# Performance work log

Hardware: AMD Instinct MI355X
Metric: run time of the kernel (lower is better)

Reference implementation:

```python
import jax, jax.numpy as jnp
import numpy as np

N_NODES = 10000
IN_CH = 128
HID = 256
OUT_CH = 1
N_EDGES_ADJ = 320000  # avg degree 32
N_TARGET = 8192


def setup_inputs() -> dict:
    key = jax.random.key(0)
    ks = jax.random.split(key, 16)
    s = 0.05  # weight scale for numerical stability
    inp = {
        'x': jax.random.normal(ks[0], (N_NODES, IN_CH), jnp.float32),
        'adj_row': jax.random.randint(ks[1], (N_EDGES_ADJ,), 0, N_NODES),
        'adj_col': jax.random.randint(ks[2], (N_EDGES_ADJ,), 0, N_NODES),
        'tar_ei': jax.random.randint(ks[3], (2, N_TARGET), 0, N_NODES),
        'beta': jnp.ones((1,), jnp.float32),
        'W1': s * jax.random.normal(ks[4], (IN_CH, HID), jnp.float32),
        'b1': jnp.zeros((HID,), jnp.float32),
        'W2': s * jax.random.normal(ks[5], (HID, HID), jnp.float32),
        'b2': jnp.zeros((HID,), jnp.float32),
        'W3': s * jax.random.normal(ks[6], (HID, HID), jnp.float32),
        'b3': jnp.zeros((HID,), jnp.float32),
        'Wij1': s * jax.random.normal(ks[7], (IN_CH, HID), jnp.float32),
        'bij1': jnp.zeros((HID,), jnp.float32),
        'Wij2': s * jax.random.normal(ks[8], (HID, HID), jnp.float32),
        'bij2': jnp.zeros((HID,), jnp.float32),
        'Wl1': s * jax.random.normal(ks[9], (HID, HID), jnp.float32),
        'bl1': jnp.zeros((HID,), jnp.float32),
        'Wl2': s * jax.random.normal(ks[10], (HID, OUT_CH), jnp.float32),
        'bl2': jnp.zeros((OUT_CH,), jnp.float32),
    }
    return inp


def reference(x, adj_row, adj_col, tar_ei, beta, W1, b1, W2, b2, W3, b3,
              Wij1, bij1, Wij2, bij2, Wl1, bl1, Wl2, bl2):
    n = x.shape[0]
    # Binary adjacency (duplicates collapse to 1, matching SparseTensor semantics)
    A = jnp.zeros((n, n), x.dtype).at[adj_row, adj_col].set(1.0)
    xi = x[tar_ei[0]]  # [E, F]
    xj = x[tar_ei[1]]  # [E, F]
    # adjoverlap: common-neighbor indicator per target edge, then spmm_add with x
    cn_mask = A[tar_ei[0]] * A[tar_ei[1]]          # [E, N]
    cn_x = cn_mask @ x                              # [E, F] sum of features over common neighbors
    # xcnlin: Linear-ReLU-Linear-ReLU-Linear (eval mode: dropout=identity, ln=identity)
    xcn = jax.nn.relu(cn_x @ W1 + b1)
    xcn = jax.nn.relu(xcn @ W2 + b2)
    xcn = xcn @ W3 + b3
    # xijlin: Linear-ReLU-Linear
    xij = jax.nn.relu((xi * xj) @ Wij1 + bij1) @ Wij2 + bij2
    # lin head: Linear-ReLU-Linear
    h = jax.nn.relu((xcn * beta + xij) @ Wl1 + bl1)
    return h @ Wl2 + bl2  # [E, 1]
```

## Files before the change

kernel.cpp:

```cpp
#include <hip/hip_runtime.h>
#include <hip/hip_bf16.h>

#define N_NODES 10000
#define IN_CH 128
#define HID 256
#define E_TAR 8192
#define N_EDGES 320000
#define WPR 320
#define WUSED 313
#define MAXCN 256
#define MASK_WORDS (N_NODES * WPR)

typedef short bf16x8 __attribute__((ext_vector_type(8)));
typedef float f32x4 __attribute__((ext_vector_type(4)));

__device__ __forceinline__ unsigned short f2bf(float f) {
  union { float f; unsigned u; } v; v.f = f;
  unsigned r = v.u + 0x7fffu + ((v.u >> 16) & 1u);
  return (unsigned short)(r >> 16);
}

__global__ void fill_zero(uint4* __restrict__ p, int n4) {
  int i = blockIdx.x * 256 + threadIdx.x;
  int stride = gridDim.x * 256;
  uint4 z = {0u, 0u, 0u, 0u};
  for (; i < n4; i += stride) p[i] = z;
}

__global__ void scatter_adj(const int* __restrict__ row, const int* __restrict__ col,
                            unsigned* __restrict__ mask) {
  int k = blockIdx.x * 256 + threadIdx.x;
  if (k < N_EDGES) {
    int r = row[k], c = col[k];
    atomicOr(&mask[(size_t)r * WPR + (c >> 5)], 1u << (c & 31));
  }
}

__global__ void cn_gather(const unsigned* __restrict__ mask, const int* __restrict__ tar,
                          const float* __restrict__ x, float* __restrict__ cnx) {
  __shared__ int cnt;
  __shared__ int list[MAXCN];
  int e = blockIdx.x;
  int i = tar[e], j = tar[E_TAR + e];
  if (threadIdx.x == 0) cnt = 0;
  __syncthreads();
  const unsigned* mi = mask + (size_t)i * WPR;
  const unsigned* mj = mask + (size_t)j * WPR;
  for (int w = threadIdx.x; w < WUSED; w += 128) {
    unsigned v = mi[w] & mj[w];
    while (v) {
      int b = __ffs(v) - 1;
      v &= v - 1;
      int pos = atomicAdd(&cnt, 1);
      if (pos < MAXCN) list[pos] = w * 32 + b;
    }
  }
  __syncthreads();
  int n = cnt; if (n > MAXCN) n = MAXCN;
  int c = threadIdx.x;
  float acc = 0.f;
  for (int t = 0; t < n; ++t) acc += x[(size_t)list[t] * IN_CH + c];
  cnx[(size_t)e * IN_CH + c] = acc;
}

__global__ __launch_bounds__(256) void gemm_mfma(
    const float* __restrict__ A, const float* __restrict__ W,
    const float* __restrict__ bias, const float* __restrict__ extra,
    const float* __restrict__ scalePtr, const int* __restrict__ tar,
    const float* __restrict__ x, int relu, int M, int N, int K,
    float* __restrict__ C)
{
  __shared__ unsigned short As[64][56];
  __shared__ unsigned short Bs[64][56];
  int m0 = blockIdx.x * 64;
  int n0 = blockIdx.y * 64;
  int tid = threadIdx.x;
  int lane = tid & 63, wv = tid >> 6;
  int wm0 = (wv >> 1) * 32, wn0 = (wv & 1) * 32;
  f32x4 acc[2][2] = {};

  int arow = tid >> 2, akb = (tid & 3) * 8;
  int bn = tid & 63, bkb = (tid >> 6) * 8;
  int gi = 0, gj = 0;
  if (tar) { gi = tar[m0 + arow]; gj = tar[E_TAR + m0 + arow]; }

  for (int k0 = 0; k0 < K; k0 += 32) {
    float av[8];
    if (tar) {
      const float* xi = x + (size_t)gi * IN_CH + k0 + akb;
      const float* xj = x + (size_t)gj * IN_CH + k0 + akb;
      #pragma unroll
      for (int u = 0; u < 8; ++u) av[u] = xi[u] * xj[u];
    } else {
      const float* ap = A + (size_t)(m0 + arow) * K + k0 + akb;
      #pragma unroll
      for (int u = 0; u < 8; ++u) av[u] = ap[u];
    }
    unsigned short abf[8];
    #pragma unroll
    for (int u = 0; u < 8; ++u) abf[u] = f2bf(av[u]);
    *(bf16x8*)&As[arow][akb] = *(bf16x8*)abf;

    unsigned short bbf[8];
    #pragma unroll
    for (int u = 0; u < 8; ++u) bbf[u] = f2bf(W[(size_t)(k0 + bkb + u) * N + n0 + bn]);
    *(bf16x8*)&Bs[bn][bkb] = *(bf16x8*)bbf;
    __syncthreads();

    int l15 = lane & 15, kq = (lane >> 4) * 8;
    bf16x8 a0 = *(bf16x8*)&As[wm0 + l15][kq];
    bf16x8 a1 = *(bf16x8*)&As[wm0 + 16 + l15][kq];
    bf16x8 b0 = *(bf16x8*)&Bs[wn0 + l15][kq];
    bf16x8 b1 = *(bf16x8*)&Bs[wn0 + 16 + l15][kq];
    acc[0][0] = __builtin_amdgcn_mfma_f32_16x16x32_bf16(a0, b0, acc[0][0], 0, 0, 0);
    acc[0][1] = __builtin_amdgcn_mfma_f32_16x16x32_bf16(a0, b1, acc[0][1], 0, 0, 0);
    acc[1][0] = __builtin_amdgcn_mfma_f32_16x16x32_bf16(a1, b0, acc[1][0], 0, 0, 0);
    acc[1][1] = __builtin_amdgcn_mfma_f32_16x16x32_bf16(a1, b1, acc[1][1], 0, 0, 0);
    __syncthreads();
  }

  float scale = scalePtr ? scalePtr[0] : 0.f;
  int l15 = lane & 15, rq = (lane >> 4) * 4;
  #pragma unroll
  for (int fm = 0; fm < 2; ++fm) {
    #pragma unroll
    for (int fn = 0; fn < 2; ++fn) {
      int cg = n0 + wn0 + fn * 16 + l15;
      float bv = bias[cg];
      #pragma unroll
      for (int i2 = 0; i2 < 4; ++i2) {
        int rg = m0 + wm0 + fm * 16 + rq + i2;
        float v = acc[fm][fn][i2] + bv;
        if (extra) v += scale * extra[(size_t)rg * N + cg];
        if (relu) v = fmaxf(v, 0.f);
        C[(size_t)rg * N + cg] = v;
      }
    }
  }
}

__global__ void final_dot(const float* __restrict__ h, const float* __restrict__ w2,
                          const float* __restrict__ b2, float* __restrict__ out) {
  int wv = threadIdx.x >> 6, lane = threadIdx.x & 63;
  int row = blockIdx.x * 4 + wv;
  const float* hr = h + (size_t)row * HID;
  float s = 0.f;
  #pragma unroll
  for (int t = 0; t < 4; ++t) s += hr[lane + 64 * t] * w2[lane + 64 * t];
  #pragma unroll
  for (int off = 32; off; off >>= 1) s += __shfl_down(s, off);
  if (lane == 0) out[row] = s + b2[0];
}

extern "C" void kernel_launch(void* const* d_in, const int* in_sizes, int n_in,
                              void* d_out, int out_size, void* d_ws, size_t ws_size,
                              hipStream_t stream) {
  const float* x      = (const float*)d_in[0];
  const int*   adj_r  = (const int*)d_in[1];
  const int*   adj_c  = (const int*)d_in[2];
  const int*   tar    = (const int*)d_in[3];
  const float* beta   = (const float*)d_in[4];
  const float* W1     = (const float*)d_in[5];
  const float* b1     = (const float*)d_in[6];
  const float* W2     = (const float*)d_in[7];
  const float* b2     = (const float*)d_in[8];
  const float* W3     = (const float*)d_in[9];
  const float* b3     = (const float*)d_in[10];
  const float* Wij1   = (const float*)d_in[11];
  const float* bij1   = (const float*)d_in[12];
  const float* Wij2   = (const float*)d_in[13];
  const float* bij2   = (const float*)d_in[14];
  const float* Wl1    = (const float*)d_in[15];
  const float* bl1    = (const float*)d_in[16];
  const float* Wl2    = (const float*)d_in[17];
  const float* bl2    = (const float*)d_in[18];

  char* ws = (char*)d_ws;
  unsigned* mask = (unsigned*)ws;
  float* bufA = (float*)(ws + (size_t)16 * 1024 * 1024);
  float* bufB = (float*)(ws + (size_t)24 * 1024 * 1024);
  float* bufC = (float*)(ws + (size_t)32 * 1024 * 1024);

  fill_zero<<<3200, 256, 0, stream>>>((uint4*)mask, MASK_WORDS / 4);
  scatter_adj<<<(N_EDGES + 255) / 256, 256, 0, stream>>>(adj_r, adj_c, mask);
  cn_gather<<<E_TAR, 128, 0, stream>>>(mask, tar, x, bufA);

  dim3 g(E_TAR / 64, HID / 64);
  gemm_mfma<<<g, 256, 0, stream>>>(bufA, W1, b1, nullptr, nullptr, nullptr, nullptr, 1, E_TAR, HID, IN_CH, bufB);
  gemm_mfma<<<g, 256, 0, stream>>>(bufB, W2, b2, nullptr, nullptr, nullptr, nullptr, 1, E_TAR, HID, HID, bufC);
  gemm_mfma<<<g, 256, 0, stream>>>(bufC, W3, b3, nullptr, nullptr, nullptr, nullptr, 0, E_TAR, HID, HID, bufB);
  gemm_mfma<<<g, 256, 0, stream>>>(nullptr, Wij1, bij1, nullptr, nullptr, tar, x, 1, E_TAR, HID, IN_CH, bufC);
  gemm_mfma<<<g, 256, 0, stream>>>(bufC, Wij2, bij2, bufB, beta, nullptr, nullptr, 0, E_TAR, HID, HID, bufA);
  gemm_mfma<<<g, 256, 0, stream>>>(bufA, Wl1, bl1, nullptr, nullptr, nullptr, nullptr, 1, E_TAR, HID, HID, bufC);
  final_dot<<<E_TAR / 4, 256, 0, stream>>>(bufC, Wl2, bl2, (float*)d_out);
}
```

Measured before the change: 88.32 us.

## Fuse MLP chain into one kernel and use CSR-based common-neighbor gathering

Replaces the six separate GEMM launches and the final dot with one fused kernel that keeps 32-row activation tiles in shared memory as bf16 across all layers. Weights are pre-transposed and converted to bf16 once per call. The common-neighbor step now builds a per-row CSR from the bitmask and probes the larger-degree node's bitmask for each neighbor of the smaller one, with one wave per target edge. This removes global round-trips of intermediate activations and the full-row bitmask scans, but adds a CSR build pass and keeps intermediates in bf16.

```diff
diff --git a/kernel.cpp b/kernel.cpp
--- a/kernel.cpp
+++ b/kernel.cpp
@@ -8,16 +8,21 @@
 #define N_EDGES 320000
 #define WPR 320
 #define WUSED 313
-#define MAXCN 256
 #define MASK_WORDS (N_NODES * WPR)
+#define CSR_MAX 128
+#define BM 32
 
 typedef short bf16x8 __attribute__((ext_vector_type(8)));
+typedef short bf16x4 __attribute__((ext_vector_type(4)));
 typedef float f32x4 __attribute__((ext_vector_type(4)));
 
 __device__ __forceinline__ unsigned short f2bf(float f) {
   union { float f; unsigned u; } v; v.f = f;
   unsigned r = v.u + 0x7fffu + ((v.u >> 16) & 1u);
   return (unsigned short)(r >> 16);
+}
+__device__ __forceinline__ float bf2f(unsigned short h) {
+  union { unsigned u; float f; } v; v.u = ((unsigned)h) << 16; return v.f;
 }
 
 __global__ void fill_zero(uint4* __restrict__ p, int n4) {
@@ -36,120 +41,282 @@
   }
 }
 
-__global__ void cn_gather(const unsigned* __restrict__ mask, const int* __restrict__ tar,
-                          const float* __restrict__ x, float* __restrict__ cnx) {
-  __shared__ int cnt;
-  __shared__ int list[MAXCN];
-  int e = blockIdx.x;
-  int i = tar[e], j = tar[E_TAR + e];
-  if (threadIdx.x == 0) cnt = 0;
-  __syncthreads();
-  const unsigned* mi = mask + (size_t)i * WPR;
-  const unsigned* mj = mask + (size_t)j * WPR;
-  for (int w = threadIdx.x; w < WUSED; w += 128) {
-    unsigned v = mi[w] & mj[w];
+__global__ void csr_build(const unsigned* __restrict__ mask, int* __restrict__ deg,
+                          int* __restrict__ csr) {
+  int row = blockIdx.x * 4 + (threadIdx.x >> 6);
+  int lane = threadIdx.x & 63;
+  const unsigned* mr = mask + (size_t)row * WPR;
+  unsigned words[5];
+  int cnt = 0;
+  #pragma unroll
+  for (int t = 0; t < 5; ++t) {
+    int w = lane + 64 * t;
+    unsigned v = (w < WUSED) ? mr[w] : 0u;
+    words[t] = v;
+    cnt += __popc(v);
+  }
+  int pre = cnt;
+  #pragma unroll
+  for (int off = 1; off < 64; off <<= 1) {
+    int n2 = __shfl_up(pre, off);
+    if (lane >= off) pre += n2;
+  }
+  int excl = pre - cnt;
+  int total = __shfl(pre, 63);
+  if (lane == 0) deg[row] = total;
+  int p = excl;
+  int* dst = csr + (size_t)row * CSR_MAX;
+  #pragma unroll
+  for (int t = 0; t < 5; ++t) {
+    unsigned v = words[t];
+    int wbase = (lane + 64 * t) * 32;
     while (v) {
       int b = __ffs(v) - 1;
       v &= v - 1;
-      int pos = atomicAdd(&cnt, 1);
-      if (pos < MAXCN) list[pos] = w * 32 + b;
-    }
-  }
-  __syncthreads();
-  int n = cnt; if (n > MAXCN) n = MAXCN;
-  int c = threadIdx.x;
-  float acc = 0.f;
-  for (int t = 0; t < n; ++t) acc += x[(size_t)list[t] * IN_CH + c];
-  cnx[(size_t)e * IN_CH + c] = acc;
-}
-
-__global__ __launch_bounds__(256) void gemm_mfma(
-    const float* __restrict__ A, const float* __restrict__ W,
-    const float* __restrict__ bias, const float* __restrict__ extra,
-    const float* __restrict__ scalePtr, const int* __restrict__ tar,
-    const float* __restrict__ x, int relu, int M, int N, int K,
-    float* __restrict__ C)
+      if (p < CSR_MAX) dst[p] = wbase + b;
+      ++p;
+    }
+  }
+}
+
+__global__ void cn_gather_csr(const unsigned* __restrict__ mask, const int* __restrict__ deg,
+                              const int* __restrict__ csr, const int* __restrict__ tar,
+                              const float* __restrict__ x, float* __restrict__ cnx) {
+  __shared__ int lists[4][256];
+  __shared__ int cnts[4];
+  int wv = threadIdx.x >> 6, lane = threadIdx.x & 63;
+  int e = blockIdx.x * 4 + wv;
+  int i = tar[e], j = tar[E_TAR + e];
+  int di = deg[i], dj = deg[j];
+  int a = (di <= dj) ? i : j;
+  int b = (di <= dj) ? j : i;
+  int da = min(di, dj);
+  if (lane == 0) cnts[wv] = 0;
+  __syncthreads();
+  const unsigned* mb = mask + (size_t)b * WPR;
+  if (da <= CSR_MAX) {
+    const int* la = csr + (size_t)a * CSR_MAX;
+    for (int t = lane; t < da; t += 64) {
+      int n = la[t];
+      if ((mb[n >> 5] >> (n & 31)) & 1u) {
+        int p = atomicAdd(&cnts[wv], 1);
+        lists[wv][p] = n;
+      }
+    }
+  } else {
+    const unsigned* ma = mask + (size_t)a * WPR;
+    for (int w = lane; w < WUSED; w += 64) {
+      unsigned v = ma[w] & mb[w];
+      while (v) {
+        int bit = __ffs(v) - 1;
+        v &= v - 1;
+        int p = atomicAdd(&cnts[wv], 1);
+        if (p < 256) lists[wv][p] = w * 32 + bit;
+      }
+    }
+  }
+  __syncthreads();
+  int n = cnts[wv]; if (n > 256) n = 256;
+  float a0 = 0.f, a1 = 0.f;
+  for (int t = 0; t < n; ++t) {
+    const float* xr = x + (size_t)lists[wv][t] * IN_CH;
+    a0 += xr[lane];
+    a1 += xr[lane + 64];
+  }
+  cnx[(size_t)e * IN_CH + lane] = a0;
+  cnx[(size_t)e * IN_CH + 64 + lane] = a1;
+}
+
+__global__ void prep_w(const float* W1, const float* W2, const float* W3,
+                       const float* Wij1, const float* Wij2, const float* Wl1,
+                       unsigned short* wts) {
+  int bid = blockIdx.x;
+  const float* W; unsigned short* O; int K, t;
+  if      (bid <  32) { W = W1;   O = wts;          K = 128; t = bid; }
+  else if (bid <  96) { W = W2;   O = wts + 32768;  K = 256; t = bid - 32; }
+  else if (bid < 160) { W = W3;   O = wts + 98304;  K = 256; t = bid - 96; }
+  else if (bid < 192) { W = Wij1; O = wts + 163840; K = 128; t = bid - 160; }
+  else if (bid < 256) { W = Wij2; O = wts + 196608; K = 256; t = bid - 192; }
+  else                { W = Wl1;  O = wts + 262144; K = 256; t = bid - 256; }
+  const int N = 256;
+  int tpk = K / 32;
+  int tk = t % tpk, tn = t / tpk;
+  __shared__ float tile[32][33];
+  int tid = threadIdx.x;
+  int c = tid & 31, r0 = tid >> 5;
+  #pragma unroll
+  for (int rr = 0; rr < 32; rr += 8)
+    tile[r0 + rr][c] = W[(size_t)(tk * 32 + r0 + rr) * N + tn * 32 + c];
+  __syncthreads();
+  #pragma unroll
+  for (int rr = 0; rr < 32; rr += 8)
+    O[(size_t)(tn * 32 + r0 + rr) * K + tk * 32 + c] = f2bf(tile[c][r0 + rr]);
+}
+
+template<int K>
+__device__ __forceinline__ void gemm_core(const unsigned short (*A)[264],
+                                          const unsigned short* __restrict__ Wt,
+                                          int lane, int wm, int wn, f32x4* acc) {
+  int l15 = lane & 15, kg = (lane >> 4) * 8;
+  const unsigned short* wb = Wt + (size_t)(wn + l15) * K + kg;
+  bf16x8 bc[4], bn_[4];
+  #pragma unroll
+  for (int f = 0; f < 4; ++f) bc[f] = *(const bf16x8*)(wb + f * 16 * K);
+  #pragma unroll
+  for (int k0 = 0; k0 < K; k0 += 32) {
+    bf16x8 a = *(const bf16x8*)&A[wm + l15][k0 + kg];
+    if (k0 + 32 < K) {
+      #pragma unroll
+      for (int f = 0; f < 4; ++f) bn_[f] = *(const bf16x8*)(wb + f * 16 * K + k0 + 32);
+    }
+    #pragma unroll
+    for (int f = 0; f < 4; ++f)
+      acc[f] = __builtin_amdgcn_mfma_f32_16x16x32_bf16(a, bc[f], acc[f], 0, 0, 0);
+    #pragma unroll
+    for (int f = 0; f < 4; ++f) bc[f] = bn_[f];
+  }
+}
+
+__device__ __forceinline__ void epi_store(unsigned short (*dst)[264], f32x4* acc,
+                                          const float* __restrict__ bias, bool relu,
+                                          int lane, int wm, int wn) {
+  int l15 = lane & 15, rq = (lane >> 4) * 4;
+  #pragma unroll
+  for (int f = 0; f < 4; ++f) {
+    float bv = bias[wn + f * 16 + l15];
+    #pragma unroll
+    for (int i = 0; i < 4; ++i) {
+      float v = acc[f][i] + bv;
+      if (relu) v = fmaxf(v, 0.f);
+      dst[wm + rq + i][wn + f * 16 + l15] = f2bf(v);
+    }
+  }
+}
+
+__global__ __launch_bounds__(512) void fused_mlp(
+    const float* __restrict__ cn_x, const float* __restrict__ x, const int* __restrict__ tar,
+    const unsigned short* __restrict__ wts,
+    const float* __restrict__ b1, const float* __restrict__ b2, const float* __restrict__ b3,
+    const float* __restrict__ bij1, const float* __restrict__ bij2, const float* __restrict__ bl1,
+    const float* __restrict__ Wl2, const float* __restrict__ bl2,
+    const float* __restrict__ betaPtr, float* __restrict__ out)
 {
-  __shared__ unsigned short As[64][56];
-  __shared__ unsigned short Bs[64][56];
-  int m0 = blockIdx.x * 64;
-  int n0 = blockIdx.y * 64;
+  __shared__ unsigned short P[BM][264];
+  __shared__ unsigned short Q[BM][264];
+  const unsigned short* Wt1   = wts;
+  const unsigned short* Wt2   = wts + 32768;
+  const unsigned short* Wt3   = wts + 98304;
+  const unsigned short* Wtij1 = wts + 163840;
+  const unsigned short* Wtij2 = wts + 196608;
+  const unsigned short* Wtl1  = wts + 262144;
+
+  int m0 = blockIdx.x * BM;
   int tid = threadIdx.x;
   int lane = tid & 63, wv = tid >> 6;
-  int wm0 = (wv >> 1) * 32, wn0 = (wv & 1) * 32;
-  f32x4 acc[2][2] = {};
-
-  int arow = tid >> 2, akb = (tid & 3) * 8;
-  int bn = tid & 63, bkb = (tid >> 6) * 8;
-  int gi = 0, gj = 0;
-  if (tar) { gi = tar[m0 + arow]; gj = tar[E_TAR + m0 + arow]; }
-
-  for (int k0 = 0; k0 < K; k0 += 32) {
-    float av[8];
-    if (tar) {
-      const float* xi = x + (size_t)gi * IN_CH + k0 + akb;
-      const float* xj = x + (size_t)gj * IN_CH + k0 + akb;
-      #pragma unroll
-      for (int u = 0; u < 8; ++u) av[u] = xi[u] * xj[u];
-    } else {
-      const float* ap = A + (size_t)(m0 + arow) * K + k0 + akb;
-      #pragma unroll
-      for (int u = 0; u < 8; ++u) av[u] = ap[u];
-    }
-    unsigned short abf[8];
-    #pragma unroll
-    for (int u = 0; u < 8; ++u) abf[u] = f2bf(av[u]);
-    *(bf16x8*)&As[arow][akb] = *(bf16x8*)abf;
-
-    unsigned short bbf[8];
-    #pragma unroll
-    for (int u = 0; u < 8; ++u) bbf[u] = f2bf(W[(size_t)(k0 + bkb + u) * N + n0 + bn]);
-    *(bf16x8*)&Bs[bn][bkb] = *(bf16x8*)bbf;
-    __syncthreads();
-
-    int l15 = lane & 15, kq = (lane >> 4) * 8;
-    bf16x8 a0 = *(bf16x8*)&As[wm0 + l15][kq];
-    bf16x8 a1 = *(bf16x8*)&As[wm0 + 16 + l15][kq];
-    bf16x8 b0 = *(bf16x8*)&Bs[wn0 + l15][kq];
-    bf16x8 b1 = *(bf16x8*)&Bs[wn0 + 16 + l15][kq];
-    acc[0][0] = __builtin_amdgcn_mfma_f32_16x16x32_bf16(a0, b0, acc[0][0], 0, 0, 0);
-    acc[0][1] = __builtin_amdgcn_mfma_f32_16x16x32_bf16(a0, b1, acc[0][1], 0, 0, 0);
-    acc[1][0] = __builtin_amdgcn_mfma_f32_16x16x32_bf16(a1, b0, acc[1][0], 0, 0, 0);
-    acc[1][1] = __builtin_amdgcn_mfma_f32_16x16x32_bf16(a1, b1, acc[1][1], 0, 0, 0);
-    __syncthreads();
-  }
-
-  float scale = scalePtr ? scalePtr[0] : 0.f;
-  int l15 = lane & 15, rq = (lane >> 4) * 4;
-  #pragma unroll
-  for (int fm = 0; fm < 2; ++fm) {
-    #pragma unroll
-    for (int fn = 0; fn < 2; ++fn) {
-      int cg = n0 + wn0 + fn * 16 + l15;
-      float bv = bias[cg];
-      #pragma unroll
-      for (int i2 = 0; i2 < 4; ++i2) {
-        int rg = m0 + wm0 + fm * 16 + rq + i2;
-        float v = acc[fm][fn][i2] + bv;
-        if (extra) v += scale * extra[(size_t)rg * N + cg];
-        if (relu) v = fmaxf(v, 0.f);
-        C[(size_t)rg * N + cg] = v;
+  int wm = (wv >> 2) * 16;
+  int wn = (wv & 3) * 64;
+  float beta_v = betaPtr[0];
+
+  {
+    int row = tid >> 4, seg = tid & 15;
+    const float* src = cn_x + (size_t)(m0 + row) * IN_CH + seg * 8;
+    f32x4 u0 = *(const f32x4*)src, u1 = *(const f32x4*)(src + 4);
+    unsigned short tmp[8];
+    #pragma unroll
+    for (int u = 0; u < 4; ++u) { tmp[u] = f2bf(u0[u]); tmp[4 + u] = f2bf(u1[u]); }
+    *(bf16x8*)&P[row][seg * 8] = *(bf16x8*)tmp;
+  }
+  __syncthreads();
+
+  f32x4 acc[4];
+  #pragma unroll
+  for (int f = 0; f < 4; ++f) acc[f] = (f32x4){0.f, 0.f, 0.f, 0.f};
+  gemm_core<128>(P, Wt1, lane, wm, wn, acc);
+  epi_store(Q, acc, b1, true, lane, wm, wn);
+  __syncthreads();
+
+  #pragma unroll
+  for (int f = 0; f < 4; ++f) acc[f] = (f32x4){0.f, 0.f, 0.f, 0.f};
+  gemm_core<256>(Q, Wt2, lane, wm, wn, acc);
+  epi_store(P, acc, b2, true, lane, wm, wn);
+  __syncthreads();
+
+  f32x4 xcn[4];
+  #pragma unroll
+  for (int f = 0; f < 4; ++f) xcn[f] = (f32x4){0.f, 0.f, 0.f, 0.f};
+  gemm_core<256>(P, Wt3, lane, wm, wn, xcn);
+  {
+    int l15 = lane & 15;
+    #pragma unroll
+    for (int f = 0; f < 4; ++f) {
+      float bv = b3[wn + f * 16 + l15];
+      #pragma unroll
+      for (int i = 0; i < 4; ++i) xcn[f][i] += bv;
+    }
+  }
+  __syncthreads();
+
+  {
+    int row = tid >> 4, seg = tid & 15;
+    int gi = tar[m0 + row], gj = tar[E_TAR + m0 + row];
+    const float* xi = x + (size_t)gi * IN_CH + seg * 8;
+    const float* xj = x + (size_t)gj * IN_CH + seg * 8;
+    f32x4 i0 = *(const f32x4*)xi, i1 = *(const f32x4*)(xi + 4);
+    f32x4 j0 = *(const f32x4*)xj, j1 = *(const f32x4*)(xj + 4);
+    unsigned short tmp[8];
+    #pragma unroll
+    for (int u = 0; u < 4; ++u) {
+      tmp[u] = f2bf(i0[u] * j0[u]);
+      tmp[4 + u] = f2bf(i1[u] * j1[u]);
+    }
+    *(bf16x8*)&P[row][seg * 8] = *(bf16x8*)tmp;
+  }
+  __syncthreads();
+
+  #pragma unroll
+  for (int f = 0; f < 4; ++f) acc[f] = (f32x4){0.f, 0.f, 0.f, 0.f};
+  gemm_core<128>(P, Wtij1, lane, wm, wn, acc);
+  epi_store(Q, acc, bij1, true, lane, wm, wn);
+  __syncthreads();
+
+  #pragma unroll
+  for (int f = 0; f < 4; ++f) acc[f] = (f32x4){0.f, 0.f, 0.f, 0.f};
+  gemm_core<256>(Q, Wtij2, lane, wm, wn, acc);
+  {
+    int l15 = lane & 15, rq = (lane >> 4) * 4;
+    #pragma unroll
+    for (int f = 0; f < 4; ++f) {
+      float bv = bij2[wn + f * 16 + l15];
+      #pragma unroll
+      for (int i = 0; i < 4; ++i) {
+        float v = acc[f][i] + bv + beta_v * xcn[f][i];
+        P[wm + rq + i][wn + f * 16 + l15] = f2bf(v);
       }
     }
   }
-}
-
-__global__ void final_dot(const float* __restrict__ h, const float* __restrict__ w2,
-                          const float* __restrict__ b2, float* __restrict__ out) {
-  int wv = threadIdx.x >> 6, lane = threadIdx.x & 63;
-  int row = blockIdx.x * 4 + wv;
-  const float* hr = h + (size_t)row * HID;
-  float s = 0.f;
-  #pragma unroll
-  for (int t = 0; t < 4; ++t) s += hr[lane + 64 * t] * w2[lane + 64 * t];
-  #pragma unroll
-  for (int off = 32; off; off >>= 1) s += __shfl_down(s, off);
-  if (lane == 0) out[row] = s + b2[0];
+  __syncthreads();
+
+  #pragma unroll
+  for (int f = 0; f < 4; ++f) acc[f] = (f32x4){0.f, 0.f, 0.f, 0.f};
+  gemm_core<256>(P, Wtl1, lane, wm, wn, acc);
+  epi_store(Q, acc, bl1, true, lane, wm, wn);
+  __syncthreads();
+
+  {
+    f32x4 w2v = *(const f32x4*)&Wl2[lane * 4];
+    float bl2v = bl2[0];
+    #pragma unroll
+    for (int rr = 0; rr < 4; ++rr) {
+      int r = wv * 4 + rr;
+      bf16x4 q = *(const bf16x4*)&Q[r][lane * 4];
+      float s = 0.f;
+      #pragma unroll
+      for (int u = 0; u < 4; ++u) s += bf2f((unsigned short)q[u]) * w2v[u];
+      #pragma unroll
+      for (int off = 32; off; off >>= 1) s += __shfl_down(s, off);
+      if (lane == 0) out[m0 + r] = s + bl2v;
+    }
+  }
 }
 
 extern "C" void kernel_launch(void* const* d_in, const int* in_sizes, int n_in,
@@ -176,21 +343,18 @@
   const float* bl2    = (const float*)d_in[18];
 
   char* ws = (char*)d_ws;
-  unsigned* mask = (unsigned*)ws;
-  float* bufA = (float*)(ws + (size_t)16 * 1024 * 1024);
-  float* bufB = (float*)(ws + (size_t)24 * 1024 * 1024);
-  float* bufC = (float*)(ws + (size_t)32 * 1024 * 1024);
-
+  unsigned*       mask = (unsigned*)ws;
+  int*            deg  = (int*)(ws + (size_t)14 * 1024 * 1024);
+  int*            csr  = (int*)(ws + (size_t)15 * 1024 * 1024);
+  float*          cnx  = (float*)(ws + (size_t)21 * 1024 * 1024);
+  unsigned short* wts  = (unsigned short*)(ws + (size_t)26 * 1024 * 1024);
+
+  prep_w<<<320, 256, 0, stream>>>(W1, W2, W3, Wij1, Wij2, Wl1, wts);
   fill_zero<<<3200, 256, 0, stream>>>((uint4*)mask, MASK_WORDS / 4);
   scatter_adj<<<(N_EDGES + 255) / 256, 256, 0, stream>>>(adj_r, adj_c, mask);
-  cn_gather<<<E_TAR, 128, 0, stream>>>(mask, tar, x, bufA);
-
-  dim3 g(E_TAR / 64, HID / 64);
-  gemm_mfma<<<g, 256, 0, stream>>>(bufA, W1, b1, nullptr, nullptr, nullptr, nullptr, 1, E_TAR, HID, IN_CH, bufB);
-  gemm_mfma<<<g, 256, 0, stream>>>(bufB, W2, b2, nullptr, nullptr, nullptr, nullptr, 1, E_TAR, HID, HID, bufC);
-  gemm_mfma<<<g, 256, 0, stream>>>(bufC, W3, b3, nullptr, nullptr, nullptr, nullptr, 0, E_TAR, HID, HID, bufB);
-  gemm_mfma<<<g, 256, 0, stream>>>(nullptr, Wij1, bij1, nullptr, nullptr, tar, x, 1, E_TAR, HID, IN_CH, bufC);
-  gemm_mfma<<<g, 256, 0, stream>>>(bufC, Wij2, bij2, bufB, beta, nullptr, nullptr, 0, E_TAR, HID, HID, bufA);
-  gemm_mfma<<<g, 256, 0, stream>>>(bufA, Wl1, bl1, nullptr, nullptr, nullptr, nullptr, 1, E_TAR, HID, HID, bufC);
-  final_dot<<<E_TAR / 4, 256, 0, stream>>>(bufC, Wl2, bl2, (float*)d_out);
-}
+  csr_build<<<N_NODES / 4, 256, 0, stream>>>(mask, deg, csr);
+  cn_gather_csr<<<E_TAR / 4, 256, 0, stream>>>(mask, deg, csr, tar, x, cnx);
+  fused_mlp<<<E_TAR / BM, 512, 0, stream>>>(cnx, x, tar, wts,
+                                            b1, b2, b3, bij1, bij2, bl1,
+                                            Wl2, bl2, beta, (float*)d_out);
+}
```

Result: faster. 82.76 us (-6.3%).
